# Kernel optimization log

Measured on AMD Instinct MI355X. Metric: run time of the kernel, lower is better.

## Reference

```python
import jax, jax.numpy as jnp
import numpy as np

T, B, H, L = 512, 32, 512, 2  # seq_len, batch, hidden_size, num_layers (input_size == H)


def _lstm_layer(x, Wih, Whh, bih, bhh):
    """x: [T,B,D]; Wih: [4H,D]; Whh: [4H,H]; biases: [4H]. Returns [T,B,H]."""
    # Precompute input contribution for all timesteps (one big GEMM).
    x_proj = jnp.einsum('tbd,gd->tbg', x, Wih) + bih + bhh  # [T,B,4H]
    h0 = jnp.zeros((x.shape[1], H), x.dtype)
    c0 = jnp.zeros((x.shape[1], H), x.dtype)

    def step(carry, xp):
        h, c = carry
        z = xp + h @ Whh.T  # [B,4H]
        i = jax.nn.sigmoid(z[:, 0 * H:1 * H])
        f = jax.nn.sigmoid(z[:, 1 * H:2 * H])
        g = jnp.tanh(z[:, 2 * H:3 * H])
        o = jax.nn.sigmoid(z[:, 3 * H:4 * H])
        c_new = f * c + i * g
        h_new = o * jnp.tanh(c_new)
        return (h_new, c_new), h_new

    (_, _), ys = jax.lax.scan(step, (h0, c0), x_proj)
    return ys  # [T,B,H]


def setup_inputs() -> dict:
    key = jax.random.key(0)
    k1, k2, k3, k4, k5 = jax.random.split(key, 5)
    scale = 1.0 / np.sqrt(H)  # torch Linear default init range ~ U(-1/sqrt(fan_in), ...)
    return {
        'seq_inputs': jax.random.normal(k1, (T, B, H), jnp.float32),
        'W_ih': jax.random.normal(k2, (L, 4 * H, H), jnp.float32) * scale,
        'W_hh': jax.random.normal(k3, (L, 4 * H, H), jnp.float32) * scale,
        'b_ih': jax.random.normal(k4, (L, 4 * H), jnp.float32) * scale,
        'b_hh': jax.random.normal(k5, (L, 4 * H), jnp.float32) * scale,
    }


def reference(seq_inputs, W_ih, W_hh, b_ih, b_hh):
    x = seq_inputs
    for l in range(L):  # small fixed layer loop
        x = _lstm_layer(x, W_ih[l], W_hh[l], b_ih[l], b_hh[l])
    return x  # [T,B,H] last-layer hidden sequence
```

## Files before the change

### kernel.cpp

```cpp
#include <hip/hip_runtime.h>


typedef _Float16 half8_t __attribute__((ext_vector_type(8)));
typedef _Float16 half4_t __attribute__((ext_vector_type(4)));
typedef float f32x4 __attribute__((ext_vector_type(4)));
typedef unsigned int u32;
typedef unsigned short u16;

#define T_LEN 512
#define BATCH 32
#define HID 512
#define SLOT 16384
#define LW (2048 * 512)

__device__ __forceinline__ float fast_sigmoid(float x) {
  return 1.f / (1.f + __expf(-x));
}
__device__ __forceinline__ float fast_tanh(float x) {
  return 1.f - 2.f / (1.f + __expf(2.f * x));
}
__device__ __forceinline__ u32 epoch_peek(const u32* p) {
  return __hip_atomic_load(p, __ATOMIC_RELAXED, __HIP_MEMORY_SCOPE_AGENT);
}

__global__ __launch_bounds__(256) void convert_k(
    const float4* __restrict__ x,
    const float4* __restrict__ wih,
    const float4* __restrict__ whh,
    const float* __restrict__ bih, const float* __restrict__ bhh,
    half4_t* __restrict__ xh, half4_t* __restrict__ wihh, half4_t* __restrict__ whhh,
    float* __restrict__ bsum) {
  const int N4X = 2097152, N4W = 524288, TOT = N4X + 2 * N4W;
  int gid = blockIdx.x * 256 + threadIdx.x;
  for (int i = gid; i < TOT; i += gridDim.x * 256) {
    float4 v;
    half4_t* dst;
    if (i < N4X) { v = x[i]; dst = xh + i; }
    else if (i < N4X + N4W) { v = wih[i - N4X]; dst = wihh + (i - N4X); }
    else { v = whh[i - N4X - N4W]; dst = whhh + (i - N4X - N4W); }
    half4_t h;
    h[0] = (_Float16)v.x; h[1] = (_Float16)v.y; h[2] = (_Float16)v.z; h[3] = (_Float16)v.w;
    *dst = h;
  }
  if (gid < 4096) bsum[gid] = bih[gid] + bhh[gid];
}

__global__ __launch_bounds__(128, 1) void lstm_fused(
    const _Float16* __restrict__ x0h,
    const _Float16* __restrict__ wih16,
    const _Float16* __restrict__ whh16,
    const float* __restrict__ bsum,
    _Float16* h0seq,
    _Float16* h1seq,
    u32* epoch0, u32* epoch1,
    float* outf) {
  int bid = blockIdx.x;
  int layer = bid >> 6, wg = bid & 63;
  int tid = threadIdx.x;
  int ln = tid & 63;
  int q = ln >> 4, l15 = ln & 15;
  int m0 = (tid >> 6) * 16;

  const _Float16* wih_l = wih16 + (size_t)layer * LW;
  const _Float16* whh_l = whh16 + (size_t)layer * LW;
  half8_t wx[2][16], wh[2][16];
  float bv[2];
#pragma unroll
  for (int j = 0; j < 2; ++j) {
    int nl = j * 16 + l15;
    int grow = (nl >> 3) * 512 + wg * 8 + (nl & 7);
    size_t ro = (size_t)grow * 512;
#pragma unroll
    for (int kc = 0; kc < 16; ++kc) {
      wx[j][kc] = *(const half8_t*)(wih_l + ro + kc * 32 + q * 8);
      wh[j][kc] = *(const half8_t*)(whh_l + ro + kc * 32 + q * 8);
    }
    bv[j] = bsum[layer * 2048 + grow];
  }

  const _Float16* xbase = layer ? (h0seq + SLOT) : x0h;
  _Float16* hself = layer ? h1seq : h0seq;
  u32* eself = layer ? epoch1 : epoch0;

  int cb = tid >> 2;
  int cp = tid & 3;
  int col0 = wg * 8 + cp * 2;
  float cst0 = 0.f, cst1 = 0.f;

  __shared__ float Zs[4 * 297];

  for (int t = 1; t <= T_LEN; ++t) {
    const _Float16* xsrc = xbase + (size_t)(t - 1) * SLOT;
    const _Float16* hsrc = hself + (size_t)(t - 1) * SLOT;
    f32x4 acc0 = {}, acc1 = {};
    half8_t af[16];

    if (layer == 0) {
#pragma unroll
      for (int kc = 0; kc < 16; ++kc)
        af[kc] = *(const half8_t*)(xsrc + (m0 + l15) * HID + kc * 32 + q * 8);
#pragma unroll
      for (int kc = 0; kc < 16; ++kc) {
        acc0 = __builtin_amdgcn_mfma_f32_16x16x32_f16(af[kc], wx[0][kc], acc0, 0, 0, 0);
        acc1 = __builtin_amdgcn_mfma_f32_16x16x32_f16(af[kc], wx[1][kc], acc1, 0, 0, 0);
      }
      u32 tgt = 64u * (u32)(t - 1);
      while (epoch_peek(epoch0) < tgt) { __builtin_amdgcn_s_sleep(1); }
      asm volatile("" ::: "memory");
    } else {
      u32 tgt0 = 64u * (u32)t, tgt1 = 64u * (u32)(t - 1);
      while (epoch_peek(epoch0) < tgt0 || epoch_peek(epoch1) < tgt1) {
        __builtin_amdgcn_s_sleep(1);
      }
      asm volatile("" ::: "memory");
#pragma unroll
      for (int kc = 0; kc < 16; ++kc)
        af[kc] = *(const half8_t*)(xsrc + (m0 + l15) * HID + kc * 32 + q * 8);
#pragma unroll
      for (int kc = 0; kc < 16; ++kc) {
        acc0 = __builtin_amdgcn_mfma_f32_16x16x32_f16(af[kc], wx[0][kc], acc0, 0, 0, 0);
        acc1 = __builtin_amdgcn_mfma_f32_16x16x32_f16(af[kc], wx[1][kc], acc1, 0, 0, 0);
      }
    }

#pragma unroll
    for (int kc = 0; kc < 16; ++kc)
      af[kc] = *(const half8_t*)(hsrc + (m0 + l15) * HID + kc * 32 + q * 8);
#pragma unroll
    for (int kc = 0; kc < 16; ++kc) {
      acc0 = __builtin_amdgcn_mfma_f32_16x16x32_f16(af[kc], wh[0][kc], acc0, 0, 0, 0);
      acc1 = __builtin_amdgcn_mfma_f32_16x16x32_f16(af[kc], wh[1][kc], acc1, 0, 0, 0);
    }

#pragma unroll
    for (int j = 0; j < 2; ++j) {
      int nl = j * 16 + l15, g = nl >> 3, c = nl & 7;
      const f32x4& a = j ? acc1 : acc0;
#pragma unroll
      for (int r = 0; r < 4; ++r)
        Zs[g * 297 + (m0 + q * 4 + r) * 9 + c] = a[r] + bv[j];
    }
    __syncthreads();

    float h0, h1;
    {
      float zi0 = Zs[0 * 297 + cb * 9 + cp * 2], zi1 = Zs[0 * 297 + cb * 9 + cp * 2 + 1];
      float zf0 = Zs[1 * 297 + cb * 9 + cp * 2], zf1 = Zs[1 * 297 + cb * 9 + cp * 2 + 1];
      float zg0 = Zs[2 * 297 + cb * 9 + cp * 2], zg1 = Zs[2 * 297 + cb * 9 + cp * 2 + 1];
      float zo0 = Zs[3 * 297 + cb * 9 + cp * 2], zo1 = Zs[3 * 297 + cb * 9 + cp * 2 + 1];
      float i0 = fast_sigmoid(zi0), f0 = fast_sigmoid(zf0), g0 = fast_tanh(zg0), o0 = fast_sigmoid(zo0);
      float i1 = fast_sigmoid(zi1), f1 = fast_sigmoid(zf1), g1 = fast_tanh(zg1), o1 = fast_sigmoid(zo1);
      cst0 = f0 * cst0 + i0 * g0;
      cst1 = f1 * cst1 + i1 * g1;
      h0 = o0 * fast_tanh(cst0);
      h1 = o1 * fast_tanh(cst1);
      u32 hp = (u32)__builtin_bit_cast(u16, (_Float16)h0) |
               ((u32)__builtin_bit_cast(u16, (_Float16)h1) << 16);
      u32* hdst = (u32*)(hself + (size_t)t * SLOT + cb * HID + col0);
      __hip_atomic_store(hdst, hp, __ATOMIC_RELAXED, __HIP_MEMORY_SCOPE_AGENT);
    }
    __syncthreads();
    if (tid == 0)
      (void)__hip_atomic_fetch_add(eself, 1u, __ATOMIC_RELAXED, __HIP_MEMORY_SCOPE_AGENT);
    if (layer) {
      float2 o2; o2.x = h0; o2.y = h1;
      *(float2*)(outf + (size_t)(t - 1) * SLOT + cb * HID + col0) = o2;
    }
  }
}

extern "C" void kernel_launch(void* const* d_in, const int* in_sizes, int n_in,
                              void* d_out, int out_size, void* d_ws, size_t ws_size,
                              hipStream_t stream) {
  const float* x = (const float*)d_in[0];
  const float* Wih = (const float*)d_in[1];
  const float* Whh = (const float*)d_in[2];
  const float* bih = (const float*)d_in[3];
  const float* bhh = (const float*)d_in[4];
  char* ws = (char*)d_ws;
  const size_t OFF_X0H = 0;
  const size_t OFF_H0SEQ = 16777216;
  const size_t OFF_H1SEQ = 33587200;
  const size_t OFF_WIH = 50397184;
  const size_t OFF_WHH = 54591488;
  const size_t OFF_BSUM = 58785792;
  const size_t OFF_EPOCH0 = 58802176;
  const size_t OFF_EPOCH1 = 58802432;
  const size_t TOTAL = 58802688;
  if (ws_size < TOTAL) return;
  _Float16* x0h = (_Float16*)(ws + OFF_X0H);
  _Float16* h0seq = (_Float16*)(ws + OFF_H0SEQ);
  _Float16* h1seq = (_Float16*)(ws + OFF_H1SEQ);
  _Float16* wihh = (_Float16*)(ws + OFF_WIH);
  _Float16* whhh = (_Float16*)(ws + OFF_WHH);
  float* bsum = (float*)(ws + OFF_BSUM);
  u32* epoch0 = (u32*)(ws + OFF_EPOCH0);
  u32* epoch1 = (u32*)(ws + OFF_EPOCH1);

  hipMemsetAsync(ws + OFF_EPOCH0, 0, 512, stream);
  hipMemsetAsync(ws + OFF_H0SEQ, 0, 32768, stream);
  hipMemsetAsync(ws + OFF_H1SEQ, 0, 32768, stream);
  convert_k<<<3072, 256, 0, stream>>>((const float4*)x, (const float4*)Wih,
                                      (const float4*)Whh, bih, bhh,
                                      (half4_t*)x0h, (half4_t*)wihh, (half4_t*)whhh, bsum);
  lstm_fused<<<128, 128, 0, stream>>>(x0h, wihh, whhh, bsum, h0seq, h1seq,
                                      epoch0, epoch1, (float*)d_out);
}
```

Measured before the change: 3.378 ms.

## Replace shared epoch counters with per-block step flags and reorder layer-1 waits

Result: no change. 3.316 ms (-1.8%).

```diff
diff --git a/kernel.cpp b/kernel.cpp
--- a/kernel.cpp
+++ b/kernel.cpp
@@ -19,8 +19,14 @@
 __device__ __forceinline__ float fast_tanh(float x) {
   return 1.f - 2.f / (1.f + __expf(2.f * x));
 }
-__device__ __forceinline__ u32 epoch_peek(const u32* p) {
-  return __hip_atomic_load(p, __ATOMIC_RELAXED, __HIP_MEMORY_SCOPE_AGENT);
+
+__device__ __forceinline__ void wait_flags(const u32* flags, int ln, u32 tgt, int self) {
+  for (;;) {
+    u32 v = __hip_atomic_load(flags + ln, __ATOMIC_RELAXED, __HIP_MEMORY_SCOPE_AGENT);
+    if (__all((int)(v >= tgt) | (int)(ln == self))) break;
+    __builtin_amdgcn_s_sleep(1);
+  }
+  asm volatile("" ::: "memory");
 }
 
 __global__ __launch_bounds__(256) void convert_k(
@@ -52,7 +58,7 @@
     const float* __restrict__ bsum,
     _Float16* h0seq,
     _Float16* h1seq,
-    u32* epoch0, u32* epoch1,
+    u32* flags0, u32* flags1,
     float* outf) {
   int bid = blockIdx.x;
   int layer = bid >> 6, wg = bid & 63;
@@ -80,7 +86,7 @@
 
   const _Float16* xbase = layer ? (h0seq + SLOT) : x0h;
   _Float16* hself = layer ? h1seq : h0seq;
-  u32* eself = layer ? epoch1 : epoch0;
+  u32* fself = layer ? flags1 : flags0;
 
   int cb = tid >> 2;
   int cp = tid & 3;
@@ -104,15 +110,26 @@
         acc0 = __builtin_amdgcn_mfma_f32_16x16x32_f16(af[kc], wx[0][kc], acc0, 0, 0, 0);
         acc1 = __builtin_amdgcn_mfma_f32_16x16x32_f16(af[kc], wx[1][kc], acc1, 0, 0, 0);
       }
-      u32 tgt = 64u * (u32)(t - 1);
-      while (epoch_peek(epoch0) < tgt) { __builtin_amdgcn_s_sleep(1); }
-      asm volatile("" ::: "memory");
+      if (t > 1) wait_flags(flags0, ln, (u32)(t - 1), wg);
+#pragma unroll
+      for (int kc = 0; kc < 16; ++kc)
+        af[kc] = *(const half8_t*)(hsrc + (m0 + l15) * HID + kc * 32 + q * 8);
+#pragma unroll
+      for (int kc = 0; kc < 16; ++kc) {
+        acc0 = __builtin_amdgcn_mfma_f32_16x16x32_f16(af[kc], wh[0][kc], acc0, 0, 0, 0);
+        acc1 = __builtin_amdgcn_mfma_f32_16x16x32_f16(af[kc], wh[1][kc], acc1, 0, 0, 0);
+      }
     } else {
-      u32 tgt0 = 64u * (u32)t, tgt1 = 64u * (u32)(t - 1);
-      while (epoch_peek(epoch0) < tgt0 || epoch_peek(epoch1) < tgt1) {
-        __builtin_amdgcn_s_sleep(1);
-      }
-      asm volatile("" ::: "memory");
+      if (t > 1) wait_flags(flags1, ln, (u32)(t - 1), wg);
+#pragma unroll
+      for (int kc = 0; kc < 16; ++kc)
+        af[kc] = *(const half8_t*)(hsrc + (m0 + l15) * HID + kc * 32 + q * 8);
+#pragma unroll
+      for (int kc = 0; kc < 16; ++kc) {
+        acc0 = __builtin_amdgcn_mfma_f32_16x16x32_f16(af[kc], wh[0][kc], acc0, 0, 0, 0);
+        acc1 = __builtin_amdgcn_mfma_f32_16x16x32_f16(af[kc], wh[1][kc], acc1, 0, 0, 0);
+      }
+      wait_flags(flags0, ln, (u32)t, -1);
 #pragma unroll
       for (int kc = 0; kc < 16; ++kc)
         af[kc] = *(const half8_t*)(xsrc + (m0 + l15) * HID + kc * 32 + q * 8);
@@ -121,15 +138,6 @@
         acc0 = __builtin_amdgcn_mfma_f32_16x16x32_f16(af[kc], wx[0][kc], acc0, 0, 0, 0);
         acc1 = __builtin_amdgcn_mfma_f32_16x16x32_f16(af[kc], wx[1][kc], acc1, 0, 0, 0);
       }
-    }
-
-#pragma unroll
-    for (int kc = 0; kc < 16; ++kc)
-      af[kc] = *(const half8_t*)(hsrc + (m0 + l15) * HID + kc * 32 + q * 8);
-#pragma unroll
-    for (int kc = 0; kc < 16; ++kc) {
-      acc0 = __builtin_amdgcn_mfma_f32_16x16x32_f16(af[kc], wh[0][kc], acc0, 0, 0, 0);
-      acc1 = __builtin_amdgcn_mfma_f32_16x16x32_f16(af[kc], wh[1][kc], acc1, 0, 0, 0);
     }
 
 #pragma unroll
@@ -161,7 +169,7 @@
     }
     __syncthreads();
     if (tid == 0)
-      (void)__hip_atomic_fetch_add(eself, 1u, __ATOMIC_RELAXED, __HIP_MEMORY_SCOPE_AGENT);
+      __hip_atomic_store(fself + wg, (u32)t, __ATOMIC_RELAXED, __HIP_MEMORY_SCOPE_AGENT);
     if (layer) {
       float2 o2; o2.x = h0; o2.y = h1;
       *(float2*)(outf + (size_t)(t - 1) * SLOT + cb * HID + col0) = o2;
@@ -184,8 +192,8 @@
   const size_t OFF_WIH = 50397184;
   const size_t OFF_WHH = 54591488;
   const size_t OFF_BSUM = 58785792;
-  const size_t OFF_EPOCH0 = 58802176;
-  const size_t OFF_EPOCH1 = 58802432;
+  const size_t OFF_FLAGS0 = 58802176;
+  const size_t OFF_FLAGS1 = 58802432;
   const size_t TOTAL = 58802688;
   if (ws_size < TOTAL) return;
   _Float16* x0h = (_Float16*)(ws + OFF_X0H);
@@ -194,15 +202,15 @@
   _Float16* wihh = (_Float16*)(ws + OFF_WIH);
   _Float16* whhh = (_Float16*)(ws + OFF_WHH);
   float* bsum = (float*)(ws + OFF_BSUM);
-  u32* epoch0 = (u32*)(ws + OFF_EPOCH0);
-  u32* epoch1 = (u32*)(ws + OFF_EPOCH1);
-
-  hipMemsetAsync(ws + OFF_EPOCH0, 0, 512, stream);
+  u32* flags0 = (u32*)(ws + OFF_FLAGS0);
+  u32* flags1 = (u32*)(ws + OFF_FLAGS1);
+
+  hipMemsetAsync(ws + OFF_FLAGS0, 0, 512, stream);
   hipMemsetAsync(ws + OFF_H0SEQ, 0, 32768, stream);
   hipMemsetAsync(ws + OFF_H1SEQ, 0, 32768, stream);
   convert_k<<<3072, 256, 0, stream>>>((const float4*)x, (const float4*)Wih,
                                       (const float4*)Whh, bih, bhh,
                                       (half4_t*)x0h, (half4_t*)wihh, (half4_t*)whhh, bsum);
   lstm_fused<<<128, 128, 0, stream>>>(x0h, wihh, whhh, bsum, h0seq, h1seq,
-                                      epoch0, epoch1, (float*)d_out);
-}
+                                      flags0, flags1, (float*)d_out);
+}
```
